# Kernel tuning notes

Hardware: AMD Instinct MI355X
Metric: run time of the kernel (lower is better)

The kernel has to match this reference:

```python
import jax, jax.numpy as jnp
import numpy as np

NEG_INF = -1e30
NEG_SLOPE = 0.2


def setup_inputs() -> dict:
    key = jax.random.key(0)
    k1, k2, k3, k4, k5 = jax.random.split(key, 5)
    B, N, D, H = 2, 2048, 512, 8
    k = D // H
    return {
        "x": jax.random.normal(k1, (B, N, D), dtype=jnp.float32),
        "A": jax.random.randint(k2, (B, N, N), 0, 2, dtype=jnp.int32),
        "W_proj": jax.random.normal(k3, (D, D), dtype=jnp.float32) * (1.0 / np.sqrt(D)),
        "W_att": jax.random.normal(k4, (H, 2 * k), dtype=jnp.float32) * (1.0 / np.sqrt(2 * k)),
        "b_att": jax.random.normal(k5, (H,), dtype=jnp.float32) * 0.01,
    }


def reference(x, A, W_proj, W_att, b_att):
    # x: [B, N, D_in]; A: [B, N, N]; W_proj: [D_in, D_out]; W_att: [H, 2k]; b_att: [H]
    B, N, _ = x.shape
    H, two_k = W_att.shape
    k = two_k // 2
    xp = jnp.einsum('bnd,do->bno', x, W_proj)            # [B, N, H*k]
    xh = xp.reshape(B, N, H, k).transpose(0, 2, 1, 3)    # [B, H, N, k]
    # Additive attention: score(i,j) = leaky_relu(w[:k]@x_i + w[k:]@x_j + b).
    # Decompose instead of materializing the O(N^2 * 2k) concat tensor.
    a_src = jnp.einsum('bhnk,hk->bhn', xh, W_att[:, :k])  # contribution of node i
    a_dst = jnp.einsum('bhnk,hk->bhn', xh, W_att[:, k:])  # contribution of node j
    scores = a_src[:, :, :, None] + a_dst[:, :, None, :] + b_att[None, :, None, None]
    scores = jax.nn.leaky_relu(scores, negative_slope=NEG_SLOPE)  # [B, H, N, N]
    mask = (A > 0)[:, None, :, :]
    scores = jnp.where(mask, scores, NEG_INF)
    att = jax.nn.softmax(scores, axis=-1)
    out = jax.nn.relu(jnp.einsum('bhij,bhjk->bhik', att, xh))  # [B, H, N, k]
    return out.transpose(0, 2, 1, 3).reshape(B, N, H * k)
```

## Files before the change

kernel.cpp:

```cpp
#include <hip/hip_runtime.h>
#include <cstdint>
#include <cstddef>

#define NEG_SLOPE 0.2f
#define LOG2E 1.4426950408889634f

#define BB 2
#define NN 2048
#define DD 512
#define HH 8
#define KK 64

typedef _Float16 half8 __attribute__((ext_vector_type(8)));
typedef _Float16 half4 __attribute__((ext_vector_type(4)));
typedef __fp16 fp16x2 __attribute__((ext_vector_type(2)));
typedef float floatx4 __attribute__((ext_vector_type(4)));

#define X16T_OFF  ((size_t)0)
#define WT_OFF    ((size_t)4194304)
#define XHT_OFF   ((size_t)4718592)
#define ASRC_OFF  ((size_t)8912896)
#define ADST_OFF  ((size_t)9043968)
#define ADMAX_OFF ((size_t)9175040)
#define MW_OFF    ((size_t)9183232)

__device__ __forceinline__ float fexp2(float x) {
#if __has_builtin(__builtin_amdgcn_exp2f)
    return __builtin_amdgcn_exp2f(x);
#else
    return exp2f(x);
#endif
}

#if __has_builtin(__builtin_amdgcn_global_load_lds)
#define GLL(gsrc, lbase, lane) \
    __builtin_amdgcn_global_load_lds((const __attribute__((address_space(1))) void*)(gsrc), \
                                     (__attribute__((address_space(3))) void*)(lbase), 16, 0, 0)
#else
#define GLL(gsrc, lbase, lane) \
    (*(uint4*)((char*)(lbase) + (size_t)(lane) * 16) = *(const uint4*)(gsrc))
#endif

__global__ __launch_bounds__(256) void k_mask(const int* __restrict__ A,
                                              unsigned long long* __restrict__ mwT) {
    __shared__ unsigned long long mwt[32][4];
    const int tid = threadIdx.x;
    const int w = tid >> 6, lane = tid & 63;
    const int bi = blockIdx.x;
    const int b = bi >> 9, n0 = (bi & 511) * 4;
    const int* Arow = A + ((size_t)b * NN + n0 + w) * NN + lane;
    int v[32];
#pragma unroll
    for (int c = 0; c < 32; ++c) v[c] = Arow[c * 64];
#pragma unroll
    for (int c = 0; c < 32; ++c) {
        unsigned long long m = __ballot(v[c] != 0);
        if (lane == 0) mwt[c][w] = m;
    }
    __syncthreads();
    if (tid < 128) {
        const int c = tid >> 2, rl = tid & 3;
        mwT[((size_t)b * 32 + c) * NN + n0 + rl] = mwt[c][rl];
    }
}

__global__ __launch_bounds__(256) void k_prep(const float* __restrict__ x,
                                              const float* __restrict__ Wp,
                                              _Float16* __restrict__ x16t,
                                              _Float16* __restrict__ WT) {
    __shared__ float tile[64][65];
    const int tid = threadIdx.x;
    const int bi = blockIdx.x;
    if (bi < 256) {
        const int r = tid & 15, cg = tid >> 4;
        const float* srow = x + (size_t)(bi * 16 + r) * DD;
        _Float16* obase = x16t + ((size_t)bi * 64) * 128 + r * 8;
#pragma unroll
        for (int q = 0; q < 4; ++q) {
            const int chunk = q * 16 + cg;
            float4 v0 = *(const float4*)(srow + chunk * 8);
            float4 v1 = *(const float4*)(srow + chunk * 8 + 4);
            half8 hv;
            hv[0] = (_Float16)v0.x; hv[1] = (_Float16)v0.y;
            hv[2] = (_Float16)v0.z; hv[3] = (_Float16)v0.w;
            hv[4] = (_Float16)v1.x; hv[5] = (_Float16)v1.y;
            hv[6] = (_Float16)v1.z; hv[7] = (_Float16)v1.w;
            *(half8*)(obase + (size_t)chunk * 128) = hv;
        }
    } else {
        const int wb = bi - 256;
        const int d0 = (wb >> 3) * 64, o0 = (wb & 7) * 64;
        const int r = tid >> 2, cq = tid & 3;
#pragma unroll
        for (int qq = 0; qq < 4; ++qq) {
            float4 v = *(const float4*)&Wp[(size_t)(d0 + r) * DD + o0 + cq * 16 + qq * 4];
            tile[r][cq * 16 + qq * 4 + 0] = v.x;
            tile[r][cq * 16 + qq * 4 + 1] = v.y;
            tile[r][cq * 16 + qq * 4 + 2] = v.z;
            tile[r][cq * 16 + qq * 4 + 3] = v.w;
        }
        __syncthreads();
#pragma unroll
        for (int qq = 0; qq < 2; ++qq) {
            half8 hv;
#pragma unroll
            for (int e = 0; e < 8; ++e) hv[e] = (_Float16)tile[cq * 16 + qq * 8 + e][r];
            *(half8*)&WT[(size_t)(o0 + r) * DD + d0 + cq * 16 + qq * 8] = hv;
        }
    }
}

__global__ __launch_bounds__(256) void k_proj(const _Float16* __restrict__ x16t,
                                              const _Float16* __restrict__ WT,
                                              const float* __restrict__ Watt,
                                              _Float16* __restrict__ xhT2,
                                              float* __restrict__ asrc,
                                              float* __restrict__ adst,
                                              float* __restrict__ admax) {
    __shared__ __align__(16) _Float16 bt[64 * 512];
    const int tid = threadIdx.x;
    const int bi = blockIdx.x;
    const int mtile = bi >> 3, h = bi & 7;
    const int m0 = mtile * 64;
    {
        const int cir = tid & 63, wv4 = tid >> 6;
        const char* gsrc = (const char*)(WT + (size_t)h * 64 * DD);
        char* lbase = (char*)bt;
#pragma unroll
        for (int q = 0; q < 16; ++q) {
            const int row = q * 4 + wv4;
            *(uint4*)(lbase + row * 1024 + ((cir ^ (row & 7)) * 16)) =
                *(const uint4*)(gsrc + (size_t)row * 1024 + cir * 16);
        }
    }
    __syncthreads();
    const int w = tid >> 6, l = tid & 63, li = l & 15, p = l >> 4;
    const char* bbase = (const char*)bt;
    const _Float16* abase = x16t + ((size_t)(mtile * 4 + w)) * 64 * 128 + li * 8;
    floatx4 acc[4] = {};
    for (int k0 = 0; k0 < DD; k0 += 32) {
        const int ch = (k0 >> 3) + p;
        half8 a = *(const half8*)(abase + (size_t)ch * 128);
#pragma unroll
        for (int ct = 0; ct < 4; ++ct) {
            const int row = ct * 16 + li;
            half8 bfr = *(const half8*)(bbase + row * 1024 + ((ch ^ (li & 7)) * 16));
            acc[ct] = __builtin_amdgcn_mfma_f32_16x16x32_f16(a, bfr, acc[ct], 0, 0, 0);
        }
    }
    const int b = m0 >> 11, n0m = m0 & (NN - 1);
    const int c = n0m >> 6;
    const int bh = b * HH + h;
    {
        char* tb2 = (char*)xhT2 + ((size_t)(bh * 32 + c)) * 8192;
        const int colchunk = w * 2 + (p >> 1);
        const int sub = (p & 1) * 8;
#pragma unroll
        for (int ct = 0; ct < 4; ++ct) {
            const int kk = ct * 16 + li;
            half4 hv;
#pragma unroll
            for (int r = 0; r < 4; ++r) hv[r] = (_Float16)acc[ct][r];
            *(half4*)(tb2 + kk * 128 + ((colchunk ^ (kk & 7)) << 4) + sub) = hv;
        }
    }
    float w1[4], w2[4];
#pragma unroll
    for (int ct = 0; ct < 4; ++ct) {
        w1[ct] = Watt[h * 128 + ct * 16 + li];
        w2[ct] = Watt[h * 128 + 64 + ct * 16 + li];
    }
    float mx = -1e30f;
#pragma unroll
    for (int r = 0; r < 4; ++r) {
        float s1 = 0.f, s2 = 0.f;
#pragma unroll
        for (int ct = 0; ct < 4; ++ct) { s1 += acc[ct][r] * w1[ct]; s2 += acc[ct][r] * w2[ct]; }
#pragma unroll
        for (int d = 1; d < 16; d <<= 1) { s1 += __shfl_xor(s1, d, 64); s2 += __shfl_xor(s2, d, 64); }
        mx = fmaxf(mx, s2);
        if (li == 0) {
            const int n = n0m + w * 16 + p * 4 + r;
            asrc[bh * NN + n] = s1;
            adst[bh * NN + n] = s2;
        }
    }
    mx = fmaxf(mx, __shfl_xor(mx, 16, 64));
    mx = fmaxf(mx, __shfl_xor(mx, 32, 64));
    if (l == 0) admax[bh * 128 + (mtile & 31) * 4 + w] = mx;
}

__global__ __launch_bounds__(256) void k_attn(const _Float16* __restrict__ xhT2,
                                              const float* __restrict__ asrc,
                                              const float* __restrict__ adst,
                                              const float* __restrict__ admax,
                                              const unsigned long long* __restrict__ mwT,
                                              const float* __restrict__ batt,
                                              float* __restrict__ out) {
    __shared__ __align__(16) _Float16 vt[2][2][4096];
    __shared__ float adl[2][2][64];
    __shared__ unsigned long long mwl[2][2][32];
    __shared__ float accd_s[2][16];
    __shared__ float amx_s;

    const int tid = threadIdx.x;
    const int w = tid >> 6, l = tid & 63, li = l & 15, p = l >> 4;
    const int g = w & 1, wr = w >> 1;
    const int bid = blockIdx.x;
    const int bh = bid >> 6, it = bid & 63;
    const int b = bh >> 3, h = bh & (HH - 1);
    const int i0 = it * 32;

    const _Float16* vbase = xhT2 + (size_t)bh * 32 * 4096;

    {
        const int c0 = g;
#pragma unroll
        for (int q = 0; q < 4; ++q) {
            const int chunk = (wr * 4 + q) * 64 + l;
            GLL(vbase + (size_t)c0 * 4096 + chunk * 8, &vt[g][0][(wr * 4 + q) * 512], l);
        }
        if (tid < 128) adl[tid >> 6][0][tid & 63] =
            adst[bh * NN + (tid >> 6) * 64 + (tid & 63)] * LOG2E;
        if (tid < 64) mwl[tid >> 5][0][tid & 31] =
            mwT[((size_t)b * 32 + (tid >> 5)) * NN + i0 + (tid & 31)];
    }
    if (w == 0) {
        float mx = fmaxf(admax[bh * 128 + l], admax[bh * 128 + 64 + l]);
#pragma unroll
        for (int d = 1; d < 64; d <<= 1) mx = fmaxf(mx, __shfl_xor(mx, d, 64));
        if (l == 0) amx_s = mx;
    }
    __syncthreads();

    const float am = amx_s;
    const float bbv = batt[h];
    const int i = i0 + wr * 16 + li;
    const float asb = (asrc[bh * NN + i] + bbv) * LOG2E;
    const float tb = asb + am * LOG2E;
    const float Mi = fmaxf(tb, NEG_SLOPE * tb);
    floatx4 acc[4] = {};
    floatx4 accd = {};
    half8 ones;
#pragma unroll
    for (int e = 0; e < 8; ++e) ones[e] = (_Float16)1.0f;

    float radl = 0.f; unsigned long long rmw = 0;
    for (int ci = 0; ci < 16; ++ci) {
        const int buf = ci & 1;
        char* vtg = (char*)&vt[g][buf][0];
        if (ci < 15) {
            const int cn = 2 * (ci + 1) + g;
#pragma unroll
            for (int q = 0; q < 4; ++q) {
                const int chunk = (wr * 4 + q) * 64 + l;
                GLL(vbase + (size_t)cn * 4096 + chunk * 8, &vt[g][buf ^ 1][(wr * 4 + q) * 512], l);
            }
            if (tid < 128) radl = adst[bh * NN + (2 * (ci + 1) + (tid >> 6)) * 64 + (tid & 63)] * LOG2E;
            if (tid < 64)  rmw = mwT[((size_t)b * 32 + 2 * (ci + 1) + (tid >> 5)) * NN + i0 + (tid & 31)];
        }
        const unsigned long long mword = mwl[g][buf][wr * 16 + li];
#pragma unroll
        for (int js = 0; js < 2; ++js) {
            const int shbase = js * 32 + p * 8;
            float4 A0 = *(const float4*)&adl[g][buf][shbase];
            float4 A1 = *(const float4*)&adl[g][buf][shbase + 4];
            const unsigned m8 = (unsigned)(mword >> shbase) & 0xFFu;
            float sv[8] = {A0.x, A0.y, A0.z, A0.w, A1.x, A1.y, A1.z, A1.w};
            float wv[8];
#pragma unroll
            for (int e = 0; e < 8; ++e) {
                float t = asb + sv[e];
                float s = fmaxf(t, NEG_SLOPE * t);
                float ev = fexp2(s - Mi);
                wv[e] = ((m8 >> e) & 1u) ? ev : 0.f;
            }
            union { fp16x2 h2[4]; half8 h8; } u;
            u.h2[0] = __builtin_amdgcn_cvt_pkrtz(wv[0], wv[1]);
            u.h2[1] = __builtin_amdgcn_cvt_pkrtz(wv[2], wv[3]);
            u.h2[2] = __builtin_amdgcn_cvt_pkrtz(wv[4], wv[5]);
            u.h2[3] = __builtin_amdgcn_cvt_pkrtz(wv[6], wv[7]);
            const half8 af = u.h8;
            accd = __builtin_amdgcn_mfma_f32_16x16x32_f16(af, ones, accd, 0, 0, 0);
#pragma unroll
            for (int ct = 0; ct < 4; ++ct) {
                const half8 bf = *(const half8*)(vtg + (ct * 16 + li) * 128 +
                                                 (((js * 4 + p) ^ (li & 7)) << 4));
                acc[ct] = __builtin_amdgcn_mfma_f32_16x16x32_f16(af, bf, acc[ct], 0, 0, 0);
            }
        }
        if (ci < 15) {
            if (tid < 128) adl[tid >> 6][buf ^ 1][tid & 63] = radl;
            if (tid < 64)  mwl[tid >> 5][buf ^ 1][tid & 31] = rmw;
        }
        __syncthreads();
    }

    float* accs = (float*)&vt[0][0][0];
    if (g == 1) {
#pragma unroll
        for (int ct = 0; ct < 4; ++ct)
#pragma unroll
            for (int r = 0; r < 4; ++r)
                accs[(wr * 16 + p * 4 + r) * 64 + ct * 16 + li] = acc[ct][r];
        if (li == 0) {
#pragma unroll
            for (int r = 0; r < 4; ++r) accd_s[wr][p * 4 + r] = accd[r];
        }
    }
    __syncthreads();
    if (g == 0) {
#pragma unroll
        for (int r = 0; r < 4; ++r) {
            const float d = accd[r] + accd_s[wr][p * 4 + r];
            const float inv = 1.f / fmaxf(d, 1e-30f);
            const int irow = i0 + wr * 16 + p * 4 + r;
            float* orow = out + ((size_t)b * NN + irow) * DD + h * KK;
#pragma unroll
            for (int ct = 0; ct < 4; ++ct) {
                const float v = (acc[ct][r] + accs[(wr * 16 + p * 4 + r) * 64 + ct * 16 + li]) * inv;
                orow[ct * 16 + li] = fmaxf(v, 0.f);
            }
        }
    }
}

extern "C" void kernel_launch(void* const* d_in, const int* in_sizes, int n_in,
                              void* d_out, int out_size, void* d_ws, size_t ws_size,
                              hipStream_t stream) {
    const float* x    = (const float*)d_in[0];
    const int*   A    = (const int*)d_in[1];
    const float* Wp   = (const float*)d_in[2];
    const float* Watt = (const float*)d_in[3];
    const float* batt = (const float*)d_in[4];
    float* out = (float*)d_out;

    char* ws = (char*)d_ws;
    _Float16* x16t = (_Float16*)(ws + X16T_OFF);
    _Float16* WT   = (_Float16*)(ws + WT_OFF);
    _Float16* xhT2 = (_Float16*)(ws + XHT_OFF);
    float* asrc  = (float*)(ws + ASRC_OFF);
    float* adst  = (float*)(ws + ADST_OFF);
    float* admax = (float*)(ws + ADMAX_OFF);
    unsigned long long* mwT = (unsigned long long*)(ws + MW_OFF);

    k_mask<<<dim3(1024), 256, 0, stream>>>(A, mwT);
    k_prep<<<dim3(320), 256, 0, stream>>>(x, Wp, x16t, WT);
    k_proj<<<dim3(512), 256, 0, stream>>>(x16t, WT, Watt, xhT2, asrc, adst, admax);
    k_attn<<<dim3(BB * HH * 64), 256, 0, stream>>>(xhT2, asrc, adst, admax, mwT, batt, out);
}
```

Measured before the change: 56.59 us.

## Factor exponentials out of attention loop and merge mask/prep kernels

```diff
diff --git a/kernel.cpp b/kernel.cpp
--- a/kernel.cpp
+++ b/kernel.cpp
@@ -13,24 +13,16 @@
 
 typedef _Float16 half8 __attribute__((ext_vector_type(8)));
 typedef _Float16 half4 __attribute__((ext_vector_type(4)));
-typedef __fp16 fp16x2 __attribute__((ext_vector_type(2)));
+typedef _Float16 half2v __attribute__((ext_vector_type(2)));
 typedef float floatx4 __attribute__((ext_vector_type(4)));
 
 #define X16T_OFF  ((size_t)0)
 #define WT_OFF    ((size_t)4194304)
 #define XHT_OFF   ((size_t)4718592)
 #define ASRC_OFF  ((size_t)8912896)
-#define ADST_OFF  ((size_t)9043968)
+#define AF_OFF    ((size_t)9043968)
 #define ADMAX_OFF ((size_t)9175040)
 #define MW_OFF    ((size_t)9183232)
-
-__device__ __forceinline__ float fexp2(float x) {
-#if __has_builtin(__builtin_amdgcn_exp2f)
-    return __builtin_amdgcn_exp2f(x);
-#else
-    return exp2f(x);
-#endif
-}
 
 #if __has_builtin(__builtin_amdgcn_global_load_lds)
 #define GLL(gsrc, lbase, lane) \
@@ -41,40 +33,38 @@
     (*(uint4*)((char*)(lbase) + (size_t)(lane) * 16) = *(const uint4*)(gsrc))
 #endif
 
-__global__ __launch_bounds__(256) void k_mask(const int* __restrict__ A,
-                                              unsigned long long* __restrict__ mwT) {
+__global__ __launch_bounds__(256) void k_pm(const int* __restrict__ A,
+                                            const float* __restrict__ x,
+                                            const float* __restrict__ Wp,
+                                            unsigned long long* __restrict__ mwT,
+                                            _Float16* __restrict__ x16t,
+                                            _Float16* __restrict__ WT) {
+    __shared__ float tile[64][65];
     __shared__ unsigned long long mwt[32][4];
     const int tid = threadIdx.x;
-    const int w = tid >> 6, lane = tid & 63;
     const int bi = blockIdx.x;
-    const int b = bi >> 9, n0 = (bi & 511) * 4;
-    const int* Arow = A + ((size_t)b * NN + n0 + w) * NN + lane;
-    int v[32];
-#pragma unroll
-    for (int c = 0; c < 32; ++c) v[c] = Arow[c * 64];
-#pragma unroll
-    for (int c = 0; c < 32; ++c) {
-        unsigned long long m = __ballot(v[c] != 0);
-        if (lane == 0) mwt[c][w] = m;
-    }
-    __syncthreads();
-    if (tid < 128) {
-        const int c = tid >> 2, rl = tid & 3;
-        mwT[((size_t)b * 32 + c) * NN + n0 + rl] = mwt[c][rl];
-    }
-}
-
-__global__ __launch_bounds__(256) void k_prep(const float* __restrict__ x,
-                                              const float* __restrict__ Wp,
-                                              _Float16* __restrict__ x16t,
-                                              _Float16* __restrict__ WT) {
-    __shared__ float tile[64][65];
-    const int tid = threadIdx.x;
-    const int bi = blockIdx.x;
-    if (bi < 256) {
+    if (bi < 1024) {
+        const int w = tid >> 6, lane = tid & 63;
+        const int b = bi >> 9, n0 = (bi & 511) * 4;
+        const int* Arow = A + ((size_t)b * NN + n0 + w) * NN + lane;
+        int v[32];
+#pragma unroll
+        for (int c = 0; c < 32; ++c) v[c] = Arow[c * 64];
+#pragma unroll
+        for (int c = 0; c < 32; ++c) {
+            unsigned long long m = __ballot(v[c] != 0);
+            if (lane == 0) mwt[c][w] = m;
+        }
+        __syncthreads();
+        if (tid < 128) {
+            const int c = tid >> 2, rl = tid & 3;
+            mwT[((size_t)b * 32 + c) * NN + n0 + rl] = mwt[c][rl];
+        }
+    } else if (bi < 1280) {
+        const int xb = bi - 1024;
         const int r = tid & 15, cg = tid >> 4;
-        const float* srow = x + (size_t)(bi * 16 + r) * DD;
-        _Float16* obase = x16t + ((size_t)bi * 64) * 128 + r * 8;
+        const float* srow = x + (size_t)(xb * 16 + r) * DD;
+        _Float16* obase = x16t + ((size_t)xb * 64) * 128 + r * 8;
 #pragma unroll
         for (int q = 0; q < 4; ++q) {
             const int chunk = q * 16 + cg;
@@ -88,7 +78,7 @@
             *(half8*)(obase + (size_t)chunk * 128) = hv;
         }
     } else {
-        const int wb = bi - 256;
+        const int wb = bi - 1280;
         const int d0 = (wb >> 3) * 64, o0 = (wb & 7) * 64;
         const int r = tid >> 2, cq = tid & 3;
 #pragma unroll
@@ -115,7 +105,7 @@
                                               const float* __restrict__ Watt,
                                               _Float16* __restrict__ xhT2,
                                               float* __restrict__ asrc,
-                                              float* __restrict__ adst,
+                                              unsigned* __restrict__ aFg,
                                               float* __restrict__ admax) {
     __shared__ __align__(16) _Float16 bt[64 * 512];
     const int tid = threadIdx.x;
@@ -182,7 +172,11 @@
         if (li == 0) {
             const int n = n0m + w * 16 + p * 4 + r;
             asrc[bh * NN + n] = s1;
-            adst[bh * NN + n] = s2;
+            const float bj = s2 * LOG2E;
+            union { half2v h; unsigned u; } cv;
+            cv.h[0] = (_Float16)exp2f(bj);
+            cv.h[1] = (_Float16)exp2f(NEG_SLOPE * bj);
+            aFg[bh * NN + n] = cv.u;
         }
     }
     mx = fmaxf(mx, __shfl_xor(mx, 16, 64));
@@ -192,13 +186,13 @@
 
 __global__ __launch_bounds__(256) void k_attn(const _Float16* __restrict__ xhT2,
                                               const float* __restrict__ asrc,
-                                              const float* __restrict__ adst,
+                                              const unsigned* __restrict__ aFg,
                                               const float* __restrict__ admax,
                                               const unsigned long long* __restrict__ mwT,
                                               const float* __restrict__ batt,
                                               float* __restrict__ out) {
     __shared__ __align__(16) _Float16 vt[2][2][4096];
-    __shared__ float adl[2][2][64];
+    __shared__ __align__(16) unsigned aFl[2][2][64];
     __shared__ unsigned long long mwl[2][2][32];
     __shared__ float accd_s[2][16];
     __shared__ float amx_s;
@@ -220,8 +214,8 @@
             const int chunk = (wr * 4 + q) * 64 + l;
             GLL(vbase + (size_t)c0 * 4096 + chunk * 8, &vt[g][0][(wr * 4 + q) * 512], l);
         }
-        if (tid < 128) adl[tid >> 6][0][tid & 63] =
-            adst[bh * NN + (tid >> 6) * 64 + (tid & 63)] * LOG2E;
+        if (tid < 128) aFl[tid >> 6][0][tid & 63] =
+            aFg[bh * NN + (tid >> 6) * 64 + (tid & 63)];
         if (tid < 64) mwl[tid >> 5][0][tid & 31] =
             mwT[((size_t)b * 32 + (tid >> 5)) * NN + i0 + (tid & 31)];
     }
@@ -236,16 +230,19 @@
     const float am = amx_s;
     const float bbv = batt[h];
     const int i = i0 + wr * 16 + li;
-    const float asb = (asrc[bh * NN + i] + bbv) * LOG2E;
-    const float tb = asb + am * LOG2E;
+    const float ai = (asrc[bh * NN + i] + bbv) * LOG2E;
+    const float tb = ai + am * LOG2E;
     const float Mi = fmaxf(tb, NEG_SLOPE * tb);
+    half2v eh2;
+    eh2[0] = (_Float16)exp2f(ai - Mi);
+    eh2[1] = (_Float16)exp2f(NEG_SLOPE * ai - Mi);
     floatx4 acc[4] = {};
     floatx4 accd = {};
     half8 ones;
 #pragma unroll
     for (int e = 0; e < 8; ++e) ones[e] = (_Float16)1.0f;
 
-    float radl = 0.f; unsigned long long rmw = 0;
+    unsigned raF = 0; unsigned long long rmw = 0;
     for (int ci = 0; ci < 16; ++ci) {
         const int buf = ci & 1;
         char* vtg = (char*)&vt[g][buf][0];
@@ -256,31 +253,25 @@
                 const int chunk = (wr * 4 + q) * 64 + l;
                 GLL(vbase + (size_t)cn * 4096 + chunk * 8, &vt[g][buf ^ 1][(wr * 4 + q) * 512], l);
             }
-            if (tid < 128) radl = adst[bh * NN + (2 * (ci + 1) + (tid >> 6)) * 64 + (tid & 63)] * LOG2E;
+            if (tid < 128) raF = aFg[bh * NN + (2 * (ci + 1) + (tid >> 6)) * 64 + (tid & 63)];
             if (tid < 64)  rmw = mwT[((size_t)b * 32 + 2 * (ci + 1) + (tid >> 5)) * NN + i0 + (tid & 31)];
         }
         const unsigned long long mword = mwl[g][buf][wr * 16 + li];
 #pragma unroll
         for (int js = 0; js < 2; ++js) {
             const int shbase = js * 32 + p * 8;
-            float4 A0 = *(const float4*)&adl[g][buf][shbase];
-            float4 A1 = *(const float4*)&adl[g][buf][shbase + 4];
+            uint4 F0 = *(const uint4*)&aFl[g][buf][shbase];
+            uint4 F1 = *(const uint4*)&aFl[g][buf][shbase + 4];
             const unsigned m8 = (unsigned)(mword >> shbase) & 0xFFu;
-            float sv[8] = {A0.x, A0.y, A0.z, A0.w, A1.x, A1.y, A1.z, A1.w};
-            float wv[8];
+            unsigned fb[8] = {F0.x, F0.y, F0.z, F0.w, F1.x, F1.y, F1.z, F1.w};
+            half8 af;
 #pragma unroll
             for (int e = 0; e < 8; ++e) {
-                float t = asb + sv[e];
-                float s = fmaxf(t, NEG_SLOPE * t);
-                float ev = fexp2(s - Mi);
-                wv[e] = ((m8 >> e) & 1u) ? ev : 0.f;
+                union { unsigned u; half2v h; } cv; cv.u = fb[e];
+                half2v em = eh2 * cv.h;
+                _Float16 wv = em[0] > em[1] ? em[0] : em[1];
+                af[e] = ((m8 >> e) & 1u) ? wv : (_Float16)0.f;
             }
-            union { fp16x2 h2[4]; half8 h8; } u;
-            u.h2[0] = __builtin_amdgcn_cvt_pkrtz(wv[0], wv[1]);
-            u.h2[1] = __builtin_amdgcn_cvt_pkrtz(wv[2], wv[3]);
-            u.h2[2] = __builtin_amdgcn_cvt_pkrtz(wv[4], wv[5]);
-            u.h2[3] = __builtin_amdgcn_cvt_pkrtz(wv[6], wv[7]);
-            const half8 af = u.h8;
             accd = __builtin_amdgcn_mfma_f32_16x16x32_f16(af, ones, accd, 0, 0, 0);
 #pragma unroll
             for (int ct = 0; ct < 4; ++ct) {
@@ -290,7 +281,7 @@
             }
         }
         if (ci < 15) {
-            if (tid < 128) adl[tid >> 6][buf ^ 1][tid & 63] = radl;
+            if (tid < 128) aFl[tid >> 6][buf ^ 1][tid & 63] = raF;
             if (tid < 64)  mwl[tid >> 5][buf ^ 1][tid & 31] = rmw;
         }
         __syncthreads();
@@ -340,12 +331,11 @@
     _Float16* WT   = (_Float16*)(ws + WT_OFF);
     _Float16* xhT2 = (_Float16*)(ws + XHT_OFF);
     float* asrc  = (float*)(ws + ASRC_OFF);
-    float* adst  = (float*)(ws + ADST_OFF);
+    unsigned* aFg = (unsigned*)(ws + AF_OFF);
     float* admax = (float*)(ws + ADMAX_OFF);
     unsigned long long* mwT = (unsigned long long*)(ws + MW_OFF);
 
-    k_mask<<<dim3(1024), 256, 0, stream>>>(A, mwT);
-    k_prep<<<dim3(320), 256, 0, stream>>>(x, Wp, x16t, WT);
-    k_proj<<<dim3(512), 256, 0, stream>>>(x16t, WT, Watt, xhT2, asrc, adst, admax);
-    k_attn<<<dim3(BB * HH * 64), 256, 0, stream>>>(xhT2, asrc, adst, admax, mwT, batt, out);
+    k_pm<<<dim3(1344), 256, 0, stream>>>(A, x, Wp, mwT, x16t, WT);
+    k_proj<<<dim3(512), 256, 0, stream>>>(x16t, WT, Watt, xhT2, asrc, aFg, admax);
+    k_attn<<<dim3(BB * HH * 64), 256, 0, stream>>>(xhT2, asrc, aFg, admax, mwT, batt, out);
 }
```

New measurement: 50.35 us. 1.12x faster.
